# Optimization experiments

Measured on AMD Instinct MI355X. Metric: run time of the kernel, lower is better.

Reference implementation:

```python
import jax, jax.numpy as jnp
import numpy as np

B, S, D, H = 2, 2048, 1024, 16
HD = D // H  # head dim = 64


def setup_inputs() -> dict:
    key = jax.random.key(0)
    ks = jax.random.split(key, 9)
    s = 1.0 / np.sqrt(D)
    return {
        "hidden_states": jax.random.normal(ks[0], (B, S, D), dtype=jnp.float32),
        "attention_mask": jnp.zeros((B, 1, 1, S), dtype=jnp.float32),
        "Wq": jax.random.normal(ks[1], (D, D), dtype=jnp.float32) * s,
        "bq": jnp.zeros((D,), dtype=jnp.float32),
        "Wk": jax.random.normal(ks[2], (D, D), dtype=jnp.float32) * s,
        "bk": jnp.zeros((D,), dtype=jnp.float32),
        "Wv": jax.random.normal(ks[3], (D, D), dtype=jnp.float32) * s,
        "bv": jnp.zeros((D,), dtype=jnp.float32),
        "Wo": jax.random.normal(ks[4], (D, D), dtype=jnp.float32) * s,
        "bo": jnp.zeros((D,), dtype=jnp.float32),
    }


def reference(hidden_states, attention_mask, Wq, bq, Wk, bk, Wv, bv, Wo, bo):
    b, s = hidden_states.shape[:2]
    # QKV projections -> [b, h, s, hd]
    def proj(W, bias):
        y = hidden_states @ W.T + bias
        return y.reshape(b, s, H, HD).transpose(0, 2, 1, 3)
    q = proj(Wq, bq)
    k = proj(Wk, bk)
    v = proj(Wv, bv)
    scores = jnp.einsum("bhqd,bhkd->bhqk", q, k) / jnp.sqrt(jnp.float32(HD))
    scores = scores + attention_mask  # additive mask, broadcast [b,1,1,s]
    probs = jax.nn.softmax(scores, axis=-1)  # dropout p=0 (eval)
    ctx = jnp.einsum("bhqk,bhkd->bhqd", probs, v)
    ctx = ctx.transpose(0, 2, 1, 3).reshape(b, s, D)
    out = ctx @ Wo.T + bo
    return (out, probs)
```

## Files before the change

### kernel.cpp

```cpp
#include <hip/hip_runtime.h>
#include <hip/hip_bf16.h>

#define B_ 2
#define S_ 2048
#define D_ 1024
#define H_ 16
#define HD_ 64

typedef short bf16x8 __attribute__((ext_vector_type(8)));
typedef float f32x4 __attribute__((ext_vector_type(4)));

typedef __attribute__((address_space(3))) void lds_void;
typedef const __attribute__((address_space(1))) void gbl_void;

__device__ __forceinline__ f32x4 mfma16(bf16x8 a, bf16x8 b, f32x4 c) {
    return __builtin_amdgcn_mfma_f32_16x16x32_bf16(a, b, c, 0, 0, 0);
}

__device__ __forceinline__ bf16x8 ldb8(const __hip_bfloat16* p) {
    return *reinterpret_cast<const bf16x8*>(p);
}

__global__ __launch_bounds__(256) void conv_kernel(const float* __restrict__ src,
                                                   __hip_bfloat16* __restrict__ dst, int n4) {
    int i = blockIdx.x * 256 + threadIdx.x;
    if (i >= n4) return;
    float4 f = reinterpret_cast<const float4*>(src)[i];
    union { __hip_bfloat16 h[4]; ushort4 u; } cv;
    cv.h[0] = __float2bfloat16(f.x);
    cv.h[1] = __float2bfloat16(f.y);
    cv.h[2] = __float2bfloat16(f.z);
    cv.h[3] = __float2bfloat16(f.w);
    reinterpret_cast<ushort4*>(dst)[i] = cv.u;
}

template <int MODE>
__global__ __launch_bounds__(256) void gemm_bt(
    const __hip_bfloat16* __restrict__ X, const __hip_bfloat16* __restrict__ Wt,
    const float* __restrict__ bias0, const float* __restrict__ bias1,
    const float* __restrict__ bias2,
    __hip_bfloat16* __restrict__ Yq, __hip_bfloat16* __restrict__ Yk,
    __hip_bfloat16* __restrict__ Yv, float* __restrict__ Yo,
    int M, int N, int K) {
    __shared__ __hip_bfloat16 As[128 * 32];
    __shared__ __hip_bfloat16 Bs[128 * 32];

    const int ntn = N >> 7;
    const int nwg = (M >> 7) * ntn;
    const int cpx = nwg >> 3;
    const int bid = blockIdx.x;
    const int lg = (bid & 7) * cpx + (bid >> 3);
    const int tm = lg / ntn;
    const int tn = lg % ntn;
    const int t = threadIdx.x;
    const int w = t >> 6, l = t & 63, g = l >> 4, c = l & 15;
    const int wr = w >> 1, wc = w & 1;

    const int lrow16 = l >> 2;
    const int lcol = (l & 3) * 8;

    const int r0 = w * 32 + lrow16;
    const int r1 = w * 32 + 16 + lrow16;
    const size_t xg0 = (size_t)(tm * 128 + r0) * K + lcol;
    const size_t xg1 = (size_t)(tm * 128 + r1) * K + lcol;
    const size_t wg0 = (size_t)(tn * 128 + r0) * K + lcol;
    const size_t wg1 = (size_t)(tn * 128 + r1) * K + lcol;

    f32x4 acc[4][4] = {};

    for (int k0 = 0; k0 < K; k0 += 32) {
        __syncthreads();
        __builtin_amdgcn_global_load_lds((gbl_void*)(X + xg0 + k0),
                                         (lds_void*)(As + (w * 32) * 32), 16, 0, 0);
        __builtin_amdgcn_global_load_lds((gbl_void*)(X + xg1 + k0),
                                         (lds_void*)(As + (w * 32 + 16) * 32), 16, 0, 0);
        __builtin_amdgcn_global_load_lds((gbl_void*)(Wt + wg0 + k0),
                                         (lds_void*)(Bs + (w * 32) * 32), 16, 0, 0);
        __builtin_amdgcn_global_load_lds((gbl_void*)(Wt + wg1 + k0),
                                         (lds_void*)(Bs + (w * 32 + 16) * 32), 16, 0, 0);
        __syncthreads();

        bf16x8 am[4], bn[4];
#pragma unroll
        for (int mi = 0; mi < 4; ++mi) am[mi] = ldb8(&As[(wr * 64 + mi * 16 + c) * 32 + g * 8]);
#pragma unroll
        for (int ni = 0; ni < 4; ++ni) bn[ni] = ldb8(&Bs[(wc * 64 + ni * 16 + c) * 32 + g * 8]);
#pragma unroll
        for (int mi = 0; mi < 4; ++mi)
#pragma unroll
            for (int ni = 0; ni < 4; ++ni)
                acc[mi][ni] = mfma16(am[mi], bn[ni], acc[mi][ni]);
    }

#pragma unroll
    for (int mi = 0; mi < 4; ++mi) {
        const int mbase = tm * 128 + wr * 64 + mi * 16 + g * 4;
#pragma unroll
        for (int ni = 0; ni < 4; ++ni) {
            const int n = tn * 128 + wc * 64 + ni * 16 + c;
#pragma unroll
            for (int r = 0; r < 4; ++r) {
                const int mm = mbase + r;
                float v = acc[mi][ni][r];
                if (MODE == 0) {
                    const float* bp = (n < 1024) ? bias0 : (n < 2048) ? bias1 : bias2;
                    const int nn = n & 1023;
                    v += bp[nn];
                    const int b = mm >> 11, s = mm & 2047;
                    const int h = nn >> 6, hd = nn & 63;
                    const size_t bh = (size_t)(b * H_ + h);
                    const __hip_bfloat16 bvv = __float2bfloat16(v);
                    if (n < 2048) {
                        __hip_bfloat16* dst = (n < 1024) ? Yq : Yk;
                        dst[(bh * S_ + s) * HD_ + hd] = bvv;
                    } else {
                        Yv[(bh * HD_ + hd) * S_ + s] = bvv;
                    }
                } else {
                    Yo[(size_t)mm * N + n] = v + bias0[n];
                }
            }
        }
    }
}

#define STAGE_K(dstc, t8v) do {                                                   \
    const int kt_ = (t8v) * 256;                                                  \
    _Pragma("unroll")                                                             \
    for (int i_ = 0; i_ < 4; ++i_) {                                              \
        const int chunk_ = w * 4 + i_;                                            \
        const int row_ = 8 * chunk_ + (l >> 3);                                   \
        const int col_ = ((l & 7) ^ ((l >> 3) & 7)) * 8;                          \
        __builtin_amdgcn_global_load_lds(                                         \
            (gbl_void*)(Kb + (size_t)(kt_ + row_) * HD_ + col_),                  \
            (lds_void*)((dstc) + chunk_ * 1024), 16, 0, 0);                       \
    }                                                                             \
} while (0)

#define STAGE_V(dstc, t8v) do {                                                   \
    const int kt_ = (t8v) * 256;                                                  \
    _Pragma("unroll")                                                             \
    for (int i_ = 0; i_ < 4; ++i_) {                                              \
        const int chunk_ = w * 4 + i_;                                            \
        const int row_ = 2 * chunk_ + (l >> 5);                                   \
        const int col_ = ((l & 31) ^ (row_ & 7)) * 8;                             \
        __builtin_amdgcn_global_load_lds(                                         \
            (gbl_void*)(Vb + (size_t)row_ * S_ + kt_ + col_),                     \
            (lds_void*)((dstc) + chunk_ * 1024), 16, 0, 0);                       \
    }                                                                             \
} while (0)

__global__ __launch_bounds__(512, 4) void attn_kernel(
    const __hip_bfloat16* __restrict__ Qh, const __hip_bfloat16* __restrict__ Kh,
    const __hip_bfloat16* __restrict__ Vt, const float* __restrict__ mask,
    float* __restrict__ probs, __hip_bfloat16* __restrict__ ctx) {
    union SMem {
        char Kdb[2][32768];
        float Cred[8][16][68];
    };
    __shared__ SMem sm;
    __shared__ float msk[2048];
    __shared__ float sred[8][16];
    __shared__ float invsh[16];

    const int bid = blockIdx.x;
    const int lg = (bid & 7) * 512 + (bid >> 3);
    const int qt = lg & 127;
    const int bh = lg >> 7;
    const int b = bh >> 4, h = bh & 15;
    const int t = threadIdx.x;
    const int w = t >> 6, l = t & 63, g = l >> 4, c = l & 15;
    const int q0 = qt * 16;
    const int kw = 32 * w;

    const __hip_bfloat16* Qb = Qh + (size_t)bh * S_ * HD_;
    const __hip_bfloat16* Kb = Kh + (size_t)bh * S_ * HD_;
    const __hip_bfloat16* Vb = Vt + (size_t)bh * HD_ * S_;
    const float* mrow = mask + (size_t)b * S_;

    *reinterpret_cast<float4*>(&msk[t * 4]) =
        *reinterpret_cast<const float4*>(&mrow[t * 4]);

    const bf16x8 aq0 = ldb8(&Qb[(q0 + c) * HD_ + g * 8]);
    const bf16x8 aq1 = ldb8(&Qb[(q0 + c) * HD_ + 32 + g * 8]);

    unsigned int uA[8][2][2];
    float lsum = 0.f;

    STAGE_K(sm.Kdb[0], 0);
#pragma unroll
    for (int t8 = 0; t8 < 8; ++t8) {
        char* cur = sm.Kdb[t8 & 1];
        if (t8 < 7) {
            STAGE_K(sm.Kdb[(t8 & 1) ^ 1], t8 + 1);
            asm volatile("s_waitcnt vmcnt(4)" ::: "memory");
        } else {
            asm volatile("s_waitcnt vmcnt(0)" ::: "memory");
        }
        if (t8 == 0) asm volatile("s_waitcnt lgkmcnt(0)" ::: "memory");
        __builtin_amdgcn_s_barrier();
        __builtin_amdgcn_sched_barrier(0);
        const int kt = t8 * 256;
#pragma unroll
        for (int ss = 0; ss < 2; ++ss) {
            const int krow = kw + ss * 16 + c;
            const char* kb2 = cur + krow * 128;
            const int sw = (krow & 7) << 4;
            const bf16x8 k0 = *reinterpret_cast<const bf16x8*>(kb2 + ((g * 16) ^ sw));
            const bf16x8 k1 = *reinterpret_cast<const bf16x8*>(kb2 + ((64 + g * 16) ^ sw));
            f32x4 aA = {};
            aA = mfma16(k0, aq0, aA);
            aA = mfma16(k1, aq1, aA);
            const float4 mk = *reinterpret_cast<const float4*>(&msk[kt + kw + ss * 16 + g * 4]);
            const float p0 = __expf(aA[0] * 0.125f + mk.x);
            const float p1 = __expf(aA[1] * 0.125f + mk.y);
            const float p2 = __expf(aA[2] * 0.125f + mk.z);
            const float p3 = __expf(aA[3] * 0.125f + mk.w);
            lsum += (p0 + p1) + (p2 + p3);
            union { __hip_bfloat16 hh[2]; unsigned int ui; } w0, w1;
            w0.hh[0] = __float2bfloat16(p0); w0.hh[1] = __float2bfloat16(p1);
            w1.hh[0] = __float2bfloat16(p2); w1.hh[1] = __float2bfloat16(p3);
            uA[t8][ss][0] = w0.ui; uA[t8][ss][1] = w1.ui;
        }
        __builtin_amdgcn_sched_barrier(0);
        __builtin_amdgcn_s_barrier();
    }

    lsum += __shfl_xor(lsum, 16);
    lsum += __shfl_xor(lsum, 32);
    if (g == 0) sred[w][c] = lsum;
    __syncthreads();
    float tot = 0.f;
#pragma unroll
    for (int w8 = 0; w8 < 8; ++w8) tot += sred[w8][c];
    const float invA = 1.0f / tot;
    if (w == 0 && g == 0) invsh[c] = invA;

    f32x4 cacc[4] = {};
    float* prowA = probs + ((size_t)bh * S_ + q0 + c) * S_;
    const int src0 = 32 * (g & 1) + c;
    const int src1 = src0 + 16;
    const int sigma = g >> 1;
    STAGE_V(sm.Kdb[0], 0);
#pragma unroll
    for (int t8 = 0; t8 < 8; ++t8) {
        const char* cur = sm.Kdb[t8 & 1];
        if (t8 < 7) STAGE_V(sm.Kdb[(t8 & 1) ^ 1], t8 + 1);
        if (t8 == 0)      asm volatile("s_waitcnt vmcnt(4)" ::: "memory");
        else if (t8 == 7) asm volatile("s_waitcnt vmcnt(2)" ::: "memory");
        else              asm volatile("s_waitcnt vmcnt(6)" ::: "memory");
        __builtin_amdgcn_s_barrier();
        __builtin_amdgcn_sched_barrier(0);
        const int kt = t8 * 256;
#pragma unroll
        for (int ss = 0; ss < 2; ++ss) {
            f32x4 oA;
            oA[0] = __uint_as_float(uA[t8][ss][0] << 16) * invA;
            oA[1] = __uint_as_float(uA[t8][ss][0] & 0xffff0000u) * invA;
            oA[2] = __uint_as_float(uA[t8][ss][1] << 16) * invA;
            oA[3] = __uint_as_float(uA[t8][ss][1] & 0xffff0000u) * invA;
            *reinterpret_cast<f32x4*>(&prowA[kt + kw + ss * 16 + g * 4]) = oA;
        }
        union { unsigned int ui[4]; bf16x8 v; } afA;
        {
            const unsigned int x00 = __shfl(uA[t8][0][0], src0);
            const unsigned int x10 = __shfl(uA[t8][1][0], src0);
            const unsigned int x01 = __shfl(uA[t8][0][1], src0);
            const unsigned int x11 = __shfl(uA[t8][1][1], src0);
            const unsigned int x02 = __shfl(uA[t8][0][0], src1);
            const unsigned int x12 = __shfl(uA[t8][1][0], src1);
            const unsigned int x03 = __shfl(uA[t8][0][1], src1);
            const unsigned int x13 = __shfl(uA[t8][1][1], src1);
            afA.ui[0] = sigma ? x10 : x00;
            afA.ui[1] = sigma ? x11 : x01;
            afA.ui[2] = sigma ? x12 : x02;
            afA.ui[3] = sigma ? x13 : x03;
        }
#pragma unroll
        for (int n = 0; n < 4; ++n) {
            const int vrow = n * 16 + c;
            const bf16x8 bv = *reinterpret_cast<const bf16x8*>(
                cur + vrow * 512 + ((64 * w + g * 16) ^ ((vrow & 7) << 4)));
            cacc[n] = mfma16(afA.v, bv, cacc[n]);
        }
        __builtin_amdgcn_sched_barrier(0);
        __builtin_amdgcn_s_barrier();
    }

    __syncthreads();
#pragma unroll
    for (int n = 0; n < 4; ++n)
#pragma unroll
        for (int r = 0; r < 4; ++r)
            sm.Cred[w][g * 4 + r][n * 16 + c] = cacc[n][r];
    __syncthreads();
    {
        const int row = t >> 5, col2 = (t & 31) * 2;
        float a0 = 0.f, a1 = 0.f;
#pragma unroll
        for (int w8 = 0; w8 < 8; ++w8) {
            const float2 vv = *reinterpret_cast<const float2*>(&sm.Cred[w8][row][col2]);
            a0 += vv.x; a1 += vv.y;
        }
        const float fin = invsh[row];
        union { __hip_bfloat16 hh[2]; unsigned int ui; } ov;
        ov.hh[0] = __float2bfloat16(a0 * fin);
        ov.hh[1] = __float2bfloat16(a1 * fin);
        *reinterpret_cast<unsigned int*>(
            &ctx[((size_t)b * S_ + q0 + row) * D_ + h * HD_ + col2]) = ov.ui;
    }
}

extern "C" void kernel_launch(void* const* d_in, const int* in_sizes, int n_in,
                              void* d_out, int out_size, void* d_ws, size_t ws_size,
                              hipStream_t stream) {
    const float* hs   = (const float*)d_in[0];
    const float* mask = (const float*)d_in[1];
    const float* Wq   = (const float*)d_in[2];
    const float* bq   = (const float*)d_in[3];
    const float* Wk   = (const float*)d_in[4];
    const float* bk   = (const float*)d_in[5];
    const float* Wv   = (const float*)d_in[6];
    const float* bv   = (const float*)d_in[7];
    const float* Wo   = (const float*)d_in[8];
    const float* bo   = (const float*)d_in[9];

    float* out   = (float*)d_out;
    float* probs = out + (size_t)B_ * S_ * D_;

    const size_t MD = (size_t)B_ * S_ * D_;
    __hip_bfloat16* hsb   = (__hip_bfloat16*)d_ws;
    __hip_bfloat16* wqkvb = hsb + MD;
    __hip_bfloat16* wob   = wqkvb + 3u * 1024u * 1024u;
    __hip_bfloat16* Qh    = wob + (size_t)1024 * 1024;
    __hip_bfloat16* Kh    = Qh + MD;
    __hip_bfloat16* Vt    = Kh + MD;
    __hip_bfloat16* ctxb  = Vt + MD;

    conv_kernel<<<4096, 256, 0, stream>>>(hs, hsb, (int)(MD / 4));
    conv_kernel<<<1024, 256, 0, stream>>>(Wq, wqkvb, 262144);
    conv_kernel<<<1024, 256, 0, stream>>>(Wk, wqkvb + 1048576, 262144);
    conv_kernel<<<1024, 256, 0, stream>>>(Wv, wqkvb + 2097152, 262144);
    conv_kernel<<<1024, 256, 0, stream>>>(Wo, wob, 262144);

    gemm_bt<0><<<32 * 24, 256, 0, stream>>>(hsb, wqkvb, bq, bk, bv,
                                            Qh, Kh, Vt, nullptr, 4096, 3072, 1024);

    attn_kernel<<<B_ * H_ * (S_ / 16), 512, 0, stream>>>(Qh, Kh, Vt, mask, probs, ctxb);

    gemm_bt<1><<<32 * 8, 256, 0, stream>>>(ctxb, wob, bo, nullptr, nullptr,
                                           nullptr, nullptr, nullptr, out, 4096, 1024, 1024);
}
```

Baseline: 313.7 us.

## Make K/V LDS staging wave-private and drop per-iteration block barriers

The V tile staging is re-laid out so that each wave loads only the 32-key slice of V it consumes, into its own 4 KB LDS region. This matches how K staging already maps onto each wave's own rows. Because no wave reads data staged by another, the two s_barriers per iteration in both the K and V loops are removed, and each wave relies only on its own vmcnt waits. A single __syncthreads is added after the mask load, and the lsum reduction uses an explicit lgkmcnt wait plus barrier. The gain is that waves no longer stall on each other during the loops. The risk is subtle visibility or ordering issues with global_load_lds, and a narrower 64-byte row swizzle that may raise LDS bank conflicts.

```diff
diff --git a/kernel.cpp b/kernel.cpp
--- a/kernel.cpp
+++ b/kernel.cpp
@@ -137,16 +137,15 @@
     }                                                                             \
 } while (0)
 
-#define STAGE_V(dstc, t8v) do {                                                   \
-    const int kt_ = (t8v) * 256;                                                  \
+#define STAGE_VP(dstc, t8v) do {                                                  \
+    const int kb_ = ((t8v) * 256 + 32 * w) * 2;                                   \
     _Pragma("unroll")                                                             \
     for (int i_ = 0; i_ < 4; ++i_) {                                              \
-        const int chunk_ = w * 4 + i_;                                            \
-        const int row_ = 2 * chunk_ + (l >> 5);                                   \
-        const int col_ = ((l & 31) ^ (row_ & 7)) * 8;                             \
+        const int row_ = 16 * i_ + (l >> 2);                                      \
+        const int scol_ = ((l & 3) * 16) ^ ((row_ & 3) << 4);                     \
         __builtin_amdgcn_global_load_lds(                                         \
-            (gbl_void*)(Vb + (size_t)row_ * S_ + kt_ + col_),                     \
-            (lds_void*)((dstc) + chunk_ * 1024), 16, 0, 0);                       \
+            (gbl_void*)((const char*)Vb + (size_t)row_ * (S_ * 2) + kb_ + scol_), \
+            (lds_void*)((dstc) + w * 4096 + i_ * 1024), 16, 0, 0);                \
     }                                                                             \
 } while (0)
 
@@ -155,7 +154,7 @@
     const __hip_bfloat16* __restrict__ Vt, const float* __restrict__ mask,
     float* __restrict__ probs, __hip_bfloat16* __restrict__ ctx) {
     union SMem {
-        char Kdb[2][32768];
+        char KV[2][32768];
         float Cred[8][16][68];
     };
     __shared__ SMem sm;
@@ -184,21 +183,21 @@
     const bf16x8 aq0 = ldb8(&Qb[(q0 + c) * HD_ + g * 8]);
     const bf16x8 aq1 = ldb8(&Qb[(q0 + c) * HD_ + 32 + g * 8]);
 
+    __syncthreads();
+
     unsigned int uA[8][2][2];
     float lsum = 0.f;
 
-    STAGE_K(sm.Kdb[0], 0);
+    STAGE_K(sm.KV[0], 0);
 #pragma unroll
     for (int t8 = 0; t8 < 8; ++t8) {
-        char* cur = sm.Kdb[t8 & 1];
+        const char* cur = sm.KV[t8 & 1];
         if (t8 < 7) {
-            STAGE_K(sm.Kdb[(t8 & 1) ^ 1], t8 + 1);
+            STAGE_K(sm.KV[(t8 & 1) ^ 1], t8 + 1);
             asm volatile("s_waitcnt vmcnt(4)" ::: "memory");
         } else {
             asm volatile("s_waitcnt vmcnt(0)" ::: "memory");
         }
-        if (t8 == 0) asm volatile("s_waitcnt lgkmcnt(0)" ::: "memory");
-        __builtin_amdgcn_s_barrier();
         __builtin_amdgcn_sched_barrier(0);
         const int kt = t8 * 256;
 #pragma unroll
@@ -223,13 +222,14 @@
             uA[t8][ss][0] = w0.ui; uA[t8][ss][1] = w1.ui;
         }
         __builtin_amdgcn_sched_barrier(0);
-        __builtin_amdgcn_s_barrier();
     }
 
     lsum += __shfl_xor(lsum, 16);
     lsum += __shfl_xor(lsum, 32);
     if (g == 0) sred[w][c] = lsum;
-    __syncthreads();
+    asm volatile("s_waitcnt lgkmcnt(0)" ::: "memory");
+    __builtin_amdgcn_s_barrier();
+    __builtin_amdgcn_sched_barrier(0);
     float tot = 0.f;
 #pragma unroll
     for (int w8 = 0; w8 < 8; ++w8) tot += sred[w8][c];
@@ -241,15 +241,14 @@
     const int src0 = 32 * (g & 1) + c;
     const int src1 = src0 + 16;
     const int sigma = g >> 1;
-    STAGE_V(sm.Kdb[0], 0);
+    STAGE_VP(sm.KV[0], 0);
 #pragma unroll
     for (int t8 = 0; t8 < 8; ++t8) {
-        const char* cur = sm.Kdb[t8 & 1];
-        if (t8 < 7) STAGE_V(sm.Kdb[(t8 & 1) ^ 1], t8 + 1);
+        const char* curV = sm.KV[t8 & 1] + w * 4096;
+        if (t8 < 7) STAGE_VP(sm.KV[(t8 & 1) ^ 1], t8 + 1);
         if (t8 == 0)      asm volatile("s_waitcnt vmcnt(4)" ::: "memory");
         else if (t8 == 7) asm volatile("s_waitcnt vmcnt(2)" ::: "memory");
         else              asm volatile("s_waitcnt vmcnt(6)" ::: "memory");
-        __builtin_amdgcn_s_barrier();
         __builtin_amdgcn_sched_barrier(0);
         const int kt = t8 * 256;
 #pragma unroll
@@ -280,11 +279,10 @@
         for (int n = 0; n < 4; ++n) {
             const int vrow = n * 16 + c;
             const bf16x8 bv = *reinterpret_cast<const bf16x8*>(
-                cur + vrow * 512 + ((64 * w + g * 16) ^ ((vrow & 7) << 4)));
+                curV + vrow * 64 + ((g * 16) ^ ((vrow & 3) << 4)));
             cacc[n] = mfma16(afA.v, bv, cacc[n]);
         }
         __builtin_amdgcn_sched_barrier(0);
-        __builtin_amdgcn_s_barrier();
     }
 
     __syncthreads();
```

Result: no change. 309.4 us (-1.4%).
